# Kernel optimization log

Hardware: AMD Instinct MI355X
Metric: run time of the kernel (lower is better)

The kernel has to match this reference:

```python
import jax, jax.numpy as jnp
import numpy as np
import math

N, LQ, C = 4, 5440, 256
H, L, P = 8, 4, 4
D = C // H
SHAPES = [(64, 64), (32, 32), (16, 16), (8, 8)]
STARTS = [0, 4096, 5120, 5376]
LEN_IN = 5440


def setup_inputs() -> dict:
    key = jax.random.key(0)
    ks = jax.random.split(key, 12)
    s = 1.0 / math.sqrt(C)
    return {
        "query": jax.random.normal(ks[0], (N, LQ, C), jnp.float32),
        "reference_points": jax.random.uniform(ks[1], (N, LQ, L, 2), jnp.float32),
        "input_flatten": jax.random.normal(ks[2], (N, LEN_IN, C), jnp.float32),
        "input_spatial_shapes": jnp.asarray(SHAPES, jnp.int32),
        "input_level_start_index": jnp.asarray(STARTS, jnp.int32),
        "w_off": jax.random.normal(ks[3], (C, H * L * P * 2), jnp.float32) * 0.01,
        "b_off": jax.random.normal(ks[4], (H * L * P * 2,), jnp.float32) * 0.5,
        "w_attn": jax.random.normal(ks[5], (C, H * L * P), jnp.float32) * 0.01,
        "b_attn": jnp.zeros((H * L * P,), jnp.float32),
        "w_val": jax.random.normal(ks[6], (C, C), jnp.float32) * s,
        "b_val": jnp.zeros((C,), jnp.float32),
        "w_out": jax.random.normal(ks[7], (C, C), jnp.float32) * s,
        "b_out": jnp.zeros((C,), jnp.float32),
    }


def _gather_corner(lv, yi, xi, w):
    # lv: (N, h*w, H, D); yi, xi: (N, Lq, H, P) int32 -> (N, Lq, H, P, D)
    n, lq, h_, p_ = yi.shape
    idx = yi * w + xi
    idx2 = idx.transpose(0, 1, 3, 2).reshape(n, lq * p_, h_)[..., None]
    g = jnp.take_along_axis(lv, idx2, axis=1)  # (N, Lq*P, H, D)
    return g.reshape(n, lq, p_, h_, -1).transpose(0, 1, 3, 2, 4)


def _msdeform(query, reference_points, input_flatten, shapes, starts,
              w_off, b_off, w_attn, b_attn, w_val, b_val, w_out, b_out):
    n, lq, c = query.shape
    value = (input_flatten @ w_val + b_val).reshape(n, -1, H, D)
    off = (query @ w_off + b_off).reshape(n, lq, H, L, P, 2)
    attn = jax.nn.softmax((query @ w_attn + b_attn).reshape(n, lq, H, L * P), axis=-1)
    # sampling locations in [0,1], (N, Lq, H, L, P, 2)
    loc = jnp.clip(reference_points[:, :, None, :, None, :] + off, 0.0, 1.0)
    sampled = []
    for lvl, (hh, ww) in enumerate(shapes):
        s0 = starts[lvl]
        lv = value[:, s0:s0 + hh * ww]  # (N, hh*ww, H, D)
        xy = loc[:, :, :, lvl] * jnp.asarray([ww, hh], jnp.float32) - 0.5  # (N,Lq,H,P,2)
        x, y = xy[..., 0], xy[..., 1]
        x0 = jnp.floor(x)
        y0 = jnp.floor(y)
        x0i = jnp.clip(x0.astype(jnp.int32), 0, ww - 1)
        x1i = jnp.clip(x0.astype(jnp.int32) + 1, 0, ww - 1)
        y0i = jnp.clip(y0.astype(jnp.int32), 0, hh - 1)
        y1i = jnp.clip(y0.astype(jnp.int32) + 1, 0, hh - 1)
        x0f, x1f = x0i.astype(x.dtype), x1i.astype(x.dtype)
        y0f, y1f = y0i.astype(y.dtype), y1i.astype(y.dtype)
        wa = ((x1f - x) * (y1f - y))[..., None]
        wb = ((x1f - x) * (y - y0f))[..., None]
        wc = ((x - x0f) * (y1f - y))[..., None]
        wd = ((x - x0f) * (y - y0f))[..., None]
        va = _gather_corner(lv, y0i, x0i, ww)
        vb = _gather_corner(lv, y1i, x0i, ww)
        vc = _gather_corner(lv, y0i, x1i, ww)
        vd = _gather_corner(lv, y1i, x1i, ww)
        sampled.append(wa * va + wb * vb + wc * vc + wd * vd)
    sampled = jnp.concatenate(sampled, axis=3)  # (N, Lq, H, L*P, D)
    out = jnp.einsum('nqhp,nqhpd->nqhd', attn, sampled).reshape(n, lq, c)
    return out @ w_out + b_out


def reference(query, reference_points, input_flatten, input_spatial_shapes,
              input_level_start_index, w_off, b_off, w_attn, b_attn,
              w_val, b_val, w_out, b_out):
    shapes = [tuple(int(v) for v in row) for row in np.asarray(input_spatial_shapes)]
    starts = [int(v) for v in np.asarray(input_level_start_index)]
    return _msdeform(query, reference_points, input_flatten, shapes, starts,
                     w_off, b_off, w_attn, b_attn, w_val, b_val, w_out, b_out)
```

## Files before the change

### kernel.cpp

```cpp
#include <hip/hip_runtime.h>
#include <hip/hip_fp16.h>
#include <math.h>

#define C_DIM 256
#define H_DIM 8
#define L_DIM 4
#define P_DIM 4
#define LQ 5440
#define LEN_IN 5440
#define NB 4
#define M_ROWS (NB * LQ)
#define NPANEL (M_ROWS / 128)

typedef __attribute__((ext_vector_type(8))) _Float16 f16x8;
typedef __attribute__((ext_vector_type(8))) unsigned short u16x8;
typedef __attribute__((ext_vector_type(4))) float f32x4;

__device__ __forceinline__ void split_f32(float a, __half& h, __half& l) {
    h = __float2half(a);
    l = __half2float(h), l = __float2half(a - __half2float(h));
}

__device__ __forceinline__ void split2_f32(float a, __half& h, __half& l) {
    h = __float2half(a);
    l = __float2half(a - __half2float(h));
}

__global__ __launch_bounds__(256) void convert_all(const float* __restrict__ w_val,
                                                   const float* __restrict__ w_off,
                                                   const float* __restrict__ w_attn,
                                                   const float* __restrict__ w_out,
                                                   const float* __restrict__ b_off,
                                                   const float* __restrict__ b_attn,
                                                   __half* __restrict__ wv_hi, __half* __restrict__ wv_lo,
                                                   __half* __restrict__ wc_hi, __half* __restrict__ wc_lo,
                                                   __half* __restrict__ wt_hi, __half* __restrict__ wt_lo,
                                                   float* __restrict__ bc) {
    const int b = blockIdx.x, k = threadIdx.x;
    if (b < 896) {
        const float* w; __half *hi, *lo; int ncols, col, orow;
        if (b < 256)      { w = w_val;  hi = wv_hi; lo = wv_lo; ncols = 256; col = b;       orow = col; }
        else if (b < 512) { w = w_off;  hi = wc_hi; lo = wc_lo; ncols = 256; col = b - 256; orow = col; }
        else if (b < 640) { w = w_attn; hi = wc_hi; lo = wc_lo; ncols = 128; col = b - 512; orow = col + 256; }
        else              { w = w_out;  hi = wt_hi; lo = wt_lo; ncols = 256; col = b - 640; orow = col; }
        const float a = w[(size_t)k * ncols + col];
        __half h, l;
        split2_f32(a, h, l);
        hi[(size_t)orow * 256 + k] = h;
        lo[(size_t)orow * 256 + k] = l;
    } else if (b == 896) {
        bc[k] = b_off[k];
    } else {
        if (k < 128) bc[256 + k] = b_attn[k];
    }
}

template <int NC, int BN, int MINW>
__global__ __launch_bounds__(256, MINW) void gemm_f16x3(const float* __restrict__ A,
                                                        const __half* __restrict__ Bhi,
                                                        const __half* __restrict__ Blo,
                                                        const float* __restrict__ bias,
                                                        float* __restrict__ outp) {
    constexpr int NF = BN / 32;
    constexpr int BCH = BN / 64;
    constexpr int NX = NC / BN;

    __shared__ __align__(16) __half sA[2][128][32];
    __shared__ __align__(16) __half sB[2][BN][32];

    const int bid = blockIdx.x;
    const int c = bid & 7;
    const int rest = bid >> 3;
    const int x = rest % NX;
    const int yg = rest / NX;
    const int y = yg * 8 + c;
    if (y >= NPANEL) return;

    const int n0 = x * BN;
    const int row0 = y * 128;
    const int t = threadIdx.x;
    const int w = t >> 6, lane = t & 63;
    const int bm = (w >> 1) * 64, bn = (w & 1) * (BN / 2);
    const int fr = lane & 15;
    const int fc = lane >> 4;

    const int ar1 = t >> 2, ar2 = ar1 + 64;
    const int ak8 = t & 3;
    const int asw1 = (ak8 ^ ((ar1 >> 1) & 3)) * 8;
    const int asw2 = (ak8 ^ ((ar2 >> 1) & 3)) * 8;
    const int bc8 = t & 3;
    int brr[BCH], bsw[BCH];
#pragma unroll
    for (int cc = 0; cc < BCH; ++cc) {
        brr[cc] = (t >> 2) + 64 * cc;
        bsw[cc] = (bc8 ^ ((brr[cc] >> 1) & 3)) * 8;
    }

    const size_t ga1 = (size_t)(row0 + ar1) * 256 + ak8 * 8;
    const size_t ga2 = (size_t)(row0 + ar2) * 256 + ak8 * 8;
    size_t gb[BCH];
#pragma unroll
    for (int cc = 0; cc < BCH; ++cc) gb[cc] = (size_t)(n0 + brr[cc]) * 256 + bc8 * 8;

    f32x4 acc[4][NF];
#pragma unroll
    for (int m = 0; m < 4; ++m)
#pragma unroll
        for (int n = 0; n < NF; ++n)
#pragma unroll
            for (int r = 0; r < 4; ++r) acc[m][n][r] = 0.f;

    float4 pa[4];
    float4 pb[2 * BCH];
    pa[0] = *(const float4*)(A + ga1);
    pa[1] = *(const float4*)(A + ga1 + 4);
    pa[2] = *(const float4*)(A + ga2);
    pa[3] = *(const float4*)(A + ga2 + 4);
#pragma unroll
    for (int cc = 0; cc < BCH; ++cc) {
        pb[cc] = *(const float4*)(Bhi + gb[cc]);
        pb[BCH + cc] = *(const float4*)(Blo + gb[cc]);
    }

    for (int kt = 0; kt < 8; ++kt) {
        if (kt) __syncthreads();
#pragma unroll
        for (int ch = 0; ch < 2; ++ch) {
            const float4 u = pa[2 * ch], v = pa[2 * ch + 1];
            const float e[8] = {u.x, u.y, u.z, u.w, v.x, v.y, v.z, v.w};
            u16x8 Hh, Ll;
#pragma unroll
            for (int i = 0; i < 8; ++i) {
                __half h, l;
                split2_f32(e[i], h, l);
                Hh[i] = __half_as_ushort(h);
                Ll[i] = __half_as_ushort(l);
            }
            const int row = ch ? ar2 : ar1;
            const int sw = ch ? asw2 : asw1;
            *(u16x8*)&sA[0][row][sw] = Hh;
            *(u16x8*)&sA[1][row][sw] = Ll;
        }
#pragma unroll
        for (int cc = 0; cc < BCH; ++cc) {
            *(float4*)&sB[0][brr[cc]][bsw[cc]] = pb[cc];
            *(float4*)&sB[1][brr[cc]][bsw[cc]] = pb[BCH + cc];
        }
        __syncthreads();
        if (kt < 7) {
            const size_t ko = (size_t)(kt + 1) * 32;
            pa[0] = *(const float4*)(A + ga1 + ko);
            pa[1] = *(const float4*)(A + ga1 + ko + 4);
            pa[2] = *(const float4*)(A + ga2 + ko);
            pa[3] = *(const float4*)(A + ga2 + ko + 4);
#pragma unroll
            for (int cc = 0; cc < BCH; ++cc) {
                pb[cc] = *(const float4*)(Bhi + gb[cc] + ko);
                pb[BCH + cc] = *(const float4*)(Blo + gb[cc] + ko);
            }
        }

        f16x8 bhf[NF], blf[NF];
#pragma unroll
        for (int n = 0; n < NF; ++n) {
            const int rowb = bn + n * 16 + fr;
            const int swb = (fc ^ ((rowb >> 1) & 3)) * 8;
            bhf[n] = *(const f16x8*)&sB[0][rowb][swb];
            blf[n] = *(const f16x8*)&sB[1][rowb][swb];
        }
#pragma unroll
        for (int m = 0; m < 4; ++m) {
            const int rowa = bm + m * 16 + fr;
            const int swa = (fc ^ ((rowa >> 1) & 3)) * 8;
            const f16x8 ah = *(const f16x8*)&sA[0][rowa][swa];
            const f16x8 al = *(const f16x8*)&sA[1][rowa][swa];
#pragma unroll
            for (int n = 0; n < NF; ++n) {
                acc[m][n] = __builtin_amdgcn_mfma_f32_16x16x32_f16(ah, bhf[n], acc[m][n], 0, 0, 0);
                acc[m][n] = __builtin_amdgcn_mfma_f32_16x16x32_f16(al, bhf[n], acc[m][n], 0, 0, 0);
                acc[m][n] = __builtin_amdgcn_mfma_f32_16x16x32_f16(ah, blf[n], acc[m][n], 0, 0, 0);
            }
        }
    }

#pragma unroll
    for (int n = 0; n < NF; ++n) {
        const int col = n0 + bn + n * 16 + fr;
        const float bv = bias[col];
#pragma unroll
        for (int m = 0; m < 4; ++m) {
            const int row = row0 + bm + m * 16 + fc * 4;
#pragma unroll
            for (int r = 0; r < 4; ++r)
                outp[(size_t)(row + r) * NC + col] = acc[m][n][r] + bv;
        }
    }
}

__global__ __launch_bounds__(256) void sample_kernel(const float* __restrict__ value,
                                                     const float* __restrict__ ol,
                                                     const float* __restrict__ refpts,
                                                     float* __restrict__ tmp) {
    const int t = threadIdx.x;
    const int w = t >> 6, lane = t & 63;

    __shared__ __align__(16) float4 s_aw[4][128];
    __shared__ __align__(16) uint4 s_of[4][128];

    const int h = lane >> 3;
    const unsigned l16 = (unsigned)(lane * 16);

    const int bid = blockIdx.x;
    const int xcd = bid & 7;
    const int pos = bid >> 3;
    const int n = xcd >> 1;
    const int qgrp = (xcd & 1) * 340 + pos;

    const char* vbn = (const char*)value + (size_t)n * (LEN_IN * C_DIM * 4);

    for (int it = 0; it < 2; ++it) {
        const int q = n * LQ + qgrp * 8 + w * 2 + it;

#pragma unroll
        for (int s = 0; s < 2; ++s) {
            const int j = lane + 64 * s;
            const int hq = j >> 4, lp = j & 15;
            const int l = lp >> 2;
            const int ww = 64 >> l;
            int st = 0;
            if (l == 1) st = 4096;
            else if (l == 2) st = 5120;
            else if (l == 3) st = 5376;

            const float2 oxy = *(const float2*)&ol[(size_t)q * 384 + 2 * j];
            const float2 rxy = *(const float2*)&refpts[((size_t)q * L_DIM + l) * 2];

            const float fw = (float)ww;
            const float x = fminf(fmaxf(rxy.x + oxy.x, 0.f), 1.f) * fw - 0.5f;
            const float y = fminf(fmaxf(rxy.y + oxy.y, 0.f), 1.f) * fw - 0.5f;
            const int xi = (int)floorf(x);
            const int yi = (int)floorf(y);
            const int x0i = min(max(xi, 0), ww - 1);
            const int x1i = min(max(xi + 1, 0), ww - 1);
            const int y0i = min(max(yi, 0), ww - 1);
            const int y1i = min(max(yi + 1, 0), ww - 1);
            const float wx0 = (float)x1i - x, wx1 = x - (float)x0i;
            const float wy0 = (float)y1i - y, wy1 = y - (float)y0i;

            const float lg = ol[(size_t)q * 384 + 256 + j];
            float m = lg;
#pragma unroll
            for (int o = 8; o; o >>= 1) m = fmaxf(m, __shfl_xor(m, o, 16));
            const float e = expf(lg - m);
            float sm = e;
#pragma unroll
            for (int o = 8; o; o >>= 1) sm += __shfl_xor(sm, o, 16);
            const float a = e / sm;

            const int p = lp * 8 + (hq ^ (lp & 7));
            float4 aw;
            aw.x = a * (wx0 * wy0);
            aw.y = a * (wx0 * wy1);
            aw.z = a * (wx1 * wy0);
            aw.w = a * (wx1 * wy1);
            uint4 of;
            of.x = (unsigned)(st + y0i * ww + x0i) << 10;
            of.y = (unsigned)(st + y1i * ww + x0i) << 10;
            of.z = (unsigned)(st + y0i * ww + x1i) << 10;
            of.w = (unsigned)(st + y1i * ww + x1i) << 10;
            s_aw[w][p] = aw;
            s_of[w][p] = of;
        }

        float4 acc;
        acc.x = 0.f; acc.y = 0.f; acc.z = 0.f; acc.w = 0.f;
#pragma unroll
        for (int lp = 0; lp < 16; lp += 2) {
            const int p0 = lp * 8 + (h ^ (lp & 7));
            const int p1 = (lp + 1) * 8 + (h ^ ((lp + 1) & 7));
            const float4 aw0 = s_aw[w][p0];
            const uint4 of0 = s_of[w][p0];
            const float4 aw1 = s_aw[w][p1];
            const uint4 of1 = s_of[w][p1];
            const float4 v0 = *(const float4*)(vbn + (of0.x + l16));
            const float4 v1 = *(const float4*)(vbn + (of0.y + l16));
            const float4 v2 = *(const float4*)(vbn + (of0.z + l16));
            const float4 v3 = *(const float4*)(vbn + (of0.w + l16));
            const float4 u0 = *(const float4*)(vbn + (of1.x + l16));
            const float4 u1 = *(const float4*)(vbn + (of1.y + l16));
            const float4 u2 = *(const float4*)(vbn + (of1.z + l16));
            const float4 u3 = *(const float4*)(vbn + (of1.w + l16));
            acc.x += aw0.x * v0.x + aw0.y * v1.x + aw0.z * v2.x + aw0.w * v3.x;
            acc.y += aw0.x * v0.y + aw0.y * v1.y + aw0.z * v2.y + aw0.w * v3.y;
            acc.z += aw0.x * v0.z + aw0.y * v1.z + aw0.z * v2.z + aw0.w * v3.z;
            acc.w += aw0.x * v0.w + aw0.y * v1.w + aw0.z * v2.w + aw0.w * v3.w;
            acc.x += aw1.x * u0.x + aw1.y * u1.x + aw1.z * u2.x + aw1.w * u3.x;
            acc.y += aw1.x * u0.y + aw1.y * u1.y + aw1.z * u2.y + aw1.w * u3.y;
            acc.z += aw1.x * u0.z + aw1.y * u1.z + aw1.z * u2.z + aw1.w * u3.z;
            acc.w += aw1.x * u0.w + aw1.y * u1.w + aw1.z * u2.w + aw1.w * u3.w;
        }
        *(float4*)&tmp[(size_t)q * 256 + (size_t)(lane * 4)] = acc;
    }
}

extern "C" void kernel_launch(void* const* d_in, const int* in_sizes, int n_in,
                              void* d_out, int out_size, void* d_ws, size_t ws_size,
                              hipStream_t stream) {
    const float* query         = (const float*)d_in[0];
    const float* refpts        = (const float*)d_in[1];
    const float* input_flatten = (const float*)d_in[2];
    const float* w_off  = (const float*)d_in[5];
    const float* b_off  = (const float*)d_in[6];
    const float* w_attn = (const float*)d_in[7];
    const float* b_attn = (const float*)d_in[8];
    const float* w_val  = (const float*)d_in[9];
    const float* b_val  = (const float*)d_in[10];
    const float* w_out  = (const float*)d_in[11];
    const float* b_out  = (const float*)d_in[12];
    float* out = (float*)d_out;

    const size_t nr = (size_t)M_ROWS;
    float* p = (float*)d_ws;
    float* value_ws = p; p += nr * 256;
    float* ol_ws    = p; p += nr * 384;
    float* tmp_ws   = p; p += nr * 256;
    float* bc_ws    = p; p += 384;
    __half* wv_hi = (__half*)p;
    __half* wv_lo = wv_hi + 256 * 256;
    __half* wc_hi = wv_lo + 256 * 256;
    __half* wc_lo = wc_hi + 384 * 256;
    __half* wt_hi = wc_lo + 384 * 256;
    __half* wt_lo = wt_hi + 256 * 256;

    convert_all<<<898, 256, 0, stream>>>(w_val, w_off, w_attn, w_out, b_off, b_attn,
                                         wv_hi, wv_lo, wc_hi, wc_lo, wt_hi, wt_lo, bc_ws);

    const int g256 = 8 * 4 * 22;
    const int g384 = 8 * 3 * 22;

    gemm_f16x3<256, 64, 4><<<g256, 256, 0, stream>>>(input_flatten, wv_hi, wv_lo, b_val, value_ws);
    gemm_f16x3<384, 128, 2><<<g384, 256, 0, stream>>>(query, wc_hi, wc_lo, bc_ws, ol_ws);

    sample_kernel<<<M_ROWS / 8, 256, 0, stream>>>(value_ws, ol_ws, refpts, tmp_ws);

    gemm_f16x3<256, 64, 4><<<g256, 256, 0, stream>>>(tmp_ws, wt_hi, wt_lo, b_out, out);
}
```

Baseline: 140.2 us.

## Merge value and offset/attention GEMMs into one launch with uniform 64-wide tiles

Replaces the templated GEMM with a single runtime-parameterized kernel that takes two problem descriptors and dispatches on block index. The value projection and the offset/attention projection now run in one grid, which removes a launch and lets the two GEMMs fill the GPU together. The 384-column GEMM also moves from 128-wide to 64-wide tiles with higher occupancy, and the bijective XCD-aware block swizzle is dropped in favour of plain row-major tile order. The costs are runtime NC division, less A-tile reuse per block for the 384 GEMM, and possibly worse L2 locality across XCDs.

```diff
diff --git a/kernel.cpp b/kernel.cpp
--- a/kernel.cpp
+++ b/kernel.cpp
@@ -17,11 +17,6 @@
 typedef __attribute__((ext_vector_type(4))) float f32x4;
 
 __device__ __forceinline__ void split_f32(float a, __half& h, __half& l) {
-    h = __float2half(a);
-    l = __half2float(h), l = __float2half(a - __half2float(h));
-}
-
-__device__ __forceinline__ void split2_f32(float a, __half& h, __half& l) {
     h = __float2half(a);
     l = __float2half(a - __half2float(h));
 }
@@ -45,7 +40,7 @@
         else              { w = w_out;  hi = wt_hi; lo = wt_lo; ncols = 256; col = b - 640; orow = col; }
         const float a = w[(size_t)k * ncols + col];
         __half h, l;
-        split2_f32(a, h, l);
+        split_f32(a, h, l);
         hi[(size_t)orow * 256 + k] = h;
         lo[(size_t)orow * 256 + k] = l;
     } else if (b == 896) {
@@ -55,32 +50,29 @@
     }
 }
 
-template <int NC, int BN, int MINW>
-__global__ __launch_bounds__(256, MINW) void gemm_f16x3(const float* __restrict__ A,
-                                                        const __half* __restrict__ Bhi,
-                                                        const __half* __restrict__ Blo,
-                                                        const float* __restrict__ bias,
-                                                        float* __restrict__ outp) {
-    constexpr int NF = BN / 32;
-    constexpr int BCH = BN / 64;
-    constexpr int NX = NC / BN;
-
+__global__ __launch_bounds__(256, 4) void gemm_f16x3(
+    int split,
+    const float* __restrict__ A0, const __half* __restrict__ B0h, const __half* __restrict__ B0l,
+    const float* __restrict__ bias0, float* __restrict__ out0, int NC0,
+    const float* __restrict__ A1, const __half* __restrict__ B1h, const __half* __restrict__ B1l,
+    const float* __restrict__ bias1, float* __restrict__ out1, int NC1) {
     __shared__ __align__(16) __half sA[2][128][32];
-    __shared__ __align__(16) __half sB[2][BN][32];
+    __shared__ __align__(16) __half sB[2][64][32];
 
     const int bid = blockIdx.x;
-    const int c = bid & 7;
-    const int rest = bid >> 3;
-    const int x = rest % NX;
-    const int yg = rest / NX;
-    const int y = yg * 8 + c;
-    if (y >= NPANEL) return;
-
-    const int n0 = x * BN;
+    const float* A; const __half* Bhi; const __half* Blo;
+    const float* bias; float* outp; int NC, idx;
+    if (bid < split) { A = A0; Bhi = B0h; Blo = B0l; bias = bias0; outp = out0; NC = NC0; idx = bid; }
+    else             { A = A1; Bhi = B1h; Blo = B1l; bias = bias1; outp = out1; NC = NC1; idx = bid - split; }
+    const int NX = NC >> 6;
+    const int y = idx / NX;
+    const int x = idx - y * NX;
+
+    const int n0 = x * 64;
     const int row0 = y * 128;
     const int t = threadIdx.x;
     const int w = t >> 6, lane = t & 63;
-    const int bm = (w >> 1) * 64, bn = (w & 1) * (BN / 2);
+    const int bm = (w >> 1) * 64, bn = (w & 1) * 32;
     const int fr = lane & 15;
     const int fc = lane >> 4;
 
@@ -88,39 +80,30 @@
     const int ak8 = t & 3;
     const int asw1 = (ak8 ^ ((ar1 >> 1) & 3)) * 8;
     const int asw2 = (ak8 ^ ((ar2 >> 1) & 3)) * 8;
+    const int br = t >> 2;
     const int bc8 = t & 3;
-    int brr[BCH], bsw[BCH];
-#pragma unroll
-    for (int cc = 0; cc < BCH; ++cc) {
-        brr[cc] = (t >> 2) + 64 * cc;
-        bsw[cc] = (bc8 ^ ((brr[cc] >> 1) & 3)) * 8;
-    }
+    const int bsw = (bc8 ^ ((br >> 1) & 3)) * 8;
 
     const size_t ga1 = (size_t)(row0 + ar1) * 256 + ak8 * 8;
     const size_t ga2 = (size_t)(row0 + ar2) * 256 + ak8 * 8;
-    size_t gb[BCH];
-#pragma unroll
-    for (int cc = 0; cc < BCH; ++cc) gb[cc] = (size_t)(n0 + brr[cc]) * 256 + bc8 * 8;
-
-    f32x4 acc[4][NF];
+    const size_t gb  = (size_t)(n0 + br) * 256 + bc8 * 8;
+
+    f32x4 acc[4][2];
 #pragma unroll
     for (int m = 0; m < 4; ++m)
 #pragma unroll
-        for (int n = 0; n < NF; ++n)
+        for (int n = 0; n < 2; ++n)
 #pragma unroll
             for (int r = 0; r < 4; ++r) acc[m][n][r] = 0.f;
 
     float4 pa[4];
-    float4 pb[2 * BCH];
+    float4 pb[2];
     pa[0] = *(const float4*)(A + ga1);
     pa[1] = *(const float4*)(A + ga1 + 4);
     pa[2] = *(const float4*)(A + ga2);
     pa[3] = *(const float4*)(A + ga2 + 4);
-#pragma unroll
-    for (int cc = 0; cc < BCH; ++cc) {
-        pb[cc] = *(const float4*)(Bhi + gb[cc]);
-        pb[BCH + cc] = *(const float4*)(Blo + gb[cc]);
-    }
+    pb[0] = *(const float4*)(Bhi + gb);
+    pb[1] = *(const float4*)(Blo + gb);
 
     for (int kt = 0; kt < 8; ++kt) {
         if (kt) __syncthreads();
@@ -132,7 +115,7 @@
 #pragma unroll
             for (int i = 0; i < 8; ++i) {
                 __half h, l;
-                split2_f32(e[i], h, l);
+                split_f32(e[i], h, l);
                 Hh[i] = __half_as_ushort(h);
                 Ll[i] = __half_as_ushort(l);
             }
@@ -141,11 +124,8 @@
             *(u16x8*)&sA[0][row][sw] = Hh;
             *(u16x8*)&sA[1][row][sw] = Ll;
         }
-#pragma unroll
-        for (int cc = 0; cc < BCH; ++cc) {
-            *(float4*)&sB[0][brr[cc]][bsw[cc]] = pb[cc];
-            *(float4*)&sB[1][brr[cc]][bsw[cc]] = pb[BCH + cc];
-        }
+        *(float4*)&sB[0][br][bsw] = pb[0];
+        *(float4*)&sB[1][br][bsw] = pb[1];
         __syncthreads();
         if (kt < 7) {
             const size_t ko = (size_t)(kt + 1) * 32;
@@ -153,16 +133,13 @@
             pa[1] = *(const float4*)(A + ga1 + ko + 4);
             pa[2] = *(const float4*)(A + ga2 + ko);
             pa[3] = *(const float4*)(A + ga2 + ko + 4);
-#pragma unroll
-            for (int cc = 0; cc < BCH; ++cc) {
-                pb[cc] = *(const float4*)(Bhi + gb[cc] + ko);
-                pb[BCH + cc] = *(const float4*)(Blo + gb[cc] + ko);
-            }
-        }
-
-        f16x8 bhf[NF], blf[NF];
-#pragma unroll
-        for (int n = 0; n < NF; ++n) {
+            pb[0] = *(const float4*)(Bhi + gb + ko);
+            pb[1] = *(const float4*)(Blo + gb + ko);
+        }
+
+        f16x8 bhf[2], blf[2];
+#pragma unroll
+        for (int n = 0; n < 2; ++n) {
             const int rowb = bn + n * 16 + fr;
             const int swb = (fc ^ ((rowb >> 1) & 3)) * 8;
             bhf[n] = *(const f16x8*)&sB[0][rowb][swb];
@@ -175,7 +152,7 @@
             const f16x8 ah = *(const f16x8*)&sA[0][rowa][swa];
             const f16x8 al = *(const f16x8*)&sA[1][rowa][swa];
 #pragma unroll
-            for (int n = 0; n < NF; ++n) {
+            for (int n = 0; n < 2; ++n) {
                 acc[m][n] = __builtin_amdgcn_mfma_f32_16x16x32_f16(ah, bhf[n], acc[m][n], 0, 0, 0);
                 acc[m][n] = __builtin_amdgcn_mfma_f32_16x16x32_f16(al, bhf[n], acc[m][n], 0, 0, 0);
                 acc[m][n] = __builtin_amdgcn_mfma_f32_16x16x32_f16(ah, blf[n], acc[m][n], 0, 0, 0);
@@ -184,7 +161,7 @@
     }
 
 #pragma unroll
-    for (int n = 0; n < NF; ++n) {
+    for (int n = 0; n < 2; ++n) {
         const int col = n0 + bn + n * 16 + fr;
         const float bv = bias[col];
 #pragma unroll
@@ -335,13 +312,16 @@
     convert_all<<<898, 256, 0, stream>>>(w_val, w_off, w_attn, w_out, b_off, b_attn,
                                          wv_hi, wv_lo, wc_hi, wc_lo, wt_hi, wt_lo, bc_ws);
 
-    const int g256 = 8 * 4 * 22;
-    const int g384 = 8 * 3 * 22;
-
-    gemm_f16x3<256, 64, 4><<<g256, 256, 0, stream>>>(input_flatten, wv_hi, wv_lo, b_val, value_ws);
-    gemm_f16x3<384, 128, 2><<<g384, 256, 0, stream>>>(query, wc_hi, wc_lo, bc_ws, ol_ws);
+    const int GV = NPANEL * 4;
+    const int GO = NPANEL * 6;
+
+    gemm_f16x3<<<GV + GO, 256, 0, stream>>>(GV,
+        input_flatten, wv_hi, wv_lo, b_val, value_ws, 256,
+        query, wc_hi, wc_lo, bc_ws, ol_ws, 384);
 
     sample_kernel<<<M_ROWS / 8, 256, 0, stream>>>(value_ws, ol_ws, refpts, tmp_ws);
 
-    gemm_f16x3<256, 64, 4><<<g256, 256, 0, stream>>>(tmp_ws, wt_hi, wt_lo, b_out, out);
-}
+    gemm_f16x3<<<GV, 256, 0, stream>>>(GV,
+        tmp_ws, wt_hi, wt_lo, b_out, out, 256,
+        tmp_ws, wt_hi, wt_lo, b_out, out, 256);
+}
```

Result: slower. 144.7 us (+3.2%).
